# Kernel tuning notes

Hardware: AMD Instinct MI355X
Metric: run time of the kernel (lower is better)

Reference implementation:

```python
import math
import jax, jax.numpy as jnp
import numpy as np

B, T, D = 8, 2048, 512


def setup_inputs() -> dict:
    key = jax.random.key(0)
    kx, = jax.random.split(key, 1)
    x = jax.random.normal(kx, (B, T, D), dtype=jnp.float32)
    log_tau = jnp.asarray(math.log(2.0), dtype=jnp.float32)
    log_blend = jnp.asarray(math.log(0.3 / 0.7), dtype=jnp.float32)
    return {"x": x, "log_tau": log_tau, "log_blend": log_blend}


def _gelu_tanh(x):
    c = math.sqrt(2.0 / math.pi)
    return 0.5 * x * (1.0 + jnp.tanh(c * (x + 0.044715 * x * x * x)))


def reference(x, log_tau, log_blend):
    Bb, Tt, Dd = x.shape
    tau = jnp.exp(log_tau)
    alpha = jax.nn.sigmoid(log_blend)
    # F.normalize(x, dim=-1): divide by L2 norm clamped to eps=1e-12
    norm = jnp.maximum(jnp.linalg.norm(x, axis=-1, keepdims=True), 1e-12)
    x_norm = x / norm
    # cosine self-similarity [B, T, T]
    sim = jnp.einsum("btd,bsd->bts", x_norm, x_norm)
    # triu(diagonal=0) masks j >= i (current + future positions)
    causal_mask = jnp.triu(jnp.ones((Tt, Tt), dtype=bool), k=0)
    sim_causal = jnp.where(causal_mask[None, :, :], -jnp.inf, sim)
    max_sim = jnp.max(sim_causal, axis=-1)  # [B, T]; row 0 is -inf
    max_sim = jnp.nan_to_num(max_sim, nan=0.0, posinf=1.0, neginf=-1.0)
    novelty = jnp.exp(-tau * max_sim)
    scale = (1.0 - alpha + alpha * novelty)[..., None]  # [B, T, 1]
    return _gelu_tanh(x * scale)
```

## Files before the change

kernel.cpp:

```cpp
#include <hip/hip_runtime.h>

#define B_ 8
#define T_ 2048
#define D_ 512

typedef float f32x16 __attribute__((ext_vector_type(16)));
typedef __bf16 bf16x8 __attribute__((ext_vector_type(8)));

__device__ __forceinline__ unsigned encf(float f) {
    int i = __float_as_int(f);
    return (i < 0) ? ~((unsigned)i) : (((unsigned)i) | 0x80000000u);
}
__device__ __forceinline__ float decf(unsigned u) {
    unsigned b = (u & 0x80000000u) ? (u ^ 0x80000000u) : ~u;
    return __int_as_float((int)b);
}

__device__ __forceinline__ void gload_lds16(const char* g, char* l) {
    __builtin_amdgcn_global_load_lds(
        (const __attribute__((address_space(1))) unsigned int*)g,
        (__attribute__((address_space(3))) unsigned int*)l, 16, 0, 0);
}

__global__ __launch_bounds__(256) void pack_kernel(
        const float* __restrict__ x, char* __restrict__ xnp,
        unsigned* __restrict__ msim, float* __restrict__ rnorm) {
    __shared__ __attribute__((aligned(16))) char sP[32768];
    int blk = blockIdx.x;
    int t   = threadIdx.x;
    int ln  = t & 63, w = t >> 6;

#pragma unroll
    for (int q = 0; q < 8; q++) {
        int row32 = q * 4 + w;
        const float* p = x + ((size_t)blk * 32 + row32) * D_ + ln * 8;
        float4 a = *(const float4*)p;
        float4 c = *(const float4*)(p + 4);
        float ss = a.x*a.x + a.y*a.y + a.z*a.z + a.w*a.w
                 + c.x*c.x + c.y*c.y + c.z*c.z + c.w*c.w;
#pragma unroll
        for (int m = 32; m; m >>= 1) ss += __shfl_xor(ss, m);
        if (ln == 0)
            rnorm[blk * 32 + row32] = 1.0f / fmaxf(sqrtf(ss), 1e-12f);
        bf16x8 h;
        h[0] = (__bf16)a.x; h[1] = (__bf16)a.y;
        h[2] = (__bf16)a.z; h[3] = (__bf16)a.w;
        h[4] = (__bf16)c.x; h[5] = (__bf16)c.y;
        h[6] = (__bf16)c.z; h[7] = (__bf16)c.w;
        int ks = ln >> 1, hcw = ln & 1;
        int slot = row32 + hcw * 32;
        int off = ks * 1024 + ((slot * 16) ^ ((ks & 7) << 4));
        *(bf16x8*)(sP + off) = h;
    }
    if (t < 32) msim[blk * 32 + t] = encf(-1e30f);
    __syncthreads();
#pragma unroll
    for (int iq = 0; iq < 8; iq++) {
        int beta = iq * 4096 + t * 16;
        int ks = beta >> 10;
        bf16x8 v = *(const bf16x8*)(sP + ks * 1024 +
                     ((beta & 1023) ^ ((ks & 7) << 4)));
        *(bf16x8*)(xnp + (size_t)blk * 32768 + beta) = v;
    }
}

__global__ __launch_bounds__(256, 2) void simmax_kernel(
        const char* __restrict__ xnp, const float* __restrict__ rnorm,
        unsigned* __restrict__ msim) {
    __shared__ __attribute__((aligned(16))) char sB[16384];

    int bid = blockIdx.x;
    int b   = bid & 7;
    int u   = 71 - (bid >> 3);
    int i = 0, cum = 0;
    while (cum + ((i + 2) >> 1) <= u) { cum += (i + 2) >> 1; i++; }
    int j0 = 2 * (u - cum);

    int t  = threadIdx.x;
    int ln = t & 63, w = t >> 6;
    int wr = w >> 1, wc = w & 1;
    int lr = ln & 31, hc = ln >> 5;
    const float NINF = -__builtin_inff();

    const char*  gA  = xnp + (size_t)(b * 64 + i * 4 + wr * 2) * 32768;
    const float* rnc = rnorm + b * T_;

    f32x16 c00, c01, c10, c11, rm0, rm1;
#pragma unroll
    for (int r = 0; r < 16; r++) {
        c00[r] = 0.f; c01[r] = 0.f; c10[r] = 0.f; c11[r] = 0.f;
        rm0[r] = NINF; rm1[r] = NINF;
    }

    for (int jj = 0; jj < 2; jj++) {
        int j = j0 + jj;
        if (j > i) break;
        const char* gB = xnp + (size_t)(b * 64 + j * 4) * 32768;
        for (int kc = 0; kc < 8; kc++) {
            __syncthreads();
#pragma unroll
            for (int q = 0; q < 4; q++)
                gload_lds16(gB + q * 32768 + (kc * 4 + w) * 1024 + ln * 16,
                            sB + q * 4096 + w * 1024 + ln * 16);
            bf16x8 aF[2][4];
#pragma unroll
            for (int p = 0; p < 2; p++)
#pragma unroll
                for (int ks = 0; ks < 4; ks++)
                    aF[p][ks] = *(const bf16x8*)(gA + p * 32768 +
                                  (kc * 4 + ks) * 1024 + ln * 16);
            __syncthreads();
            const char* bb = sB + (wc * 2) * 4096 + ln * 16;
#pragma unroll
            for (int ks = 0; ks < 4; ks++) {
                bf16x8 b0 = *(const bf16x8*)(bb + ks * 1024);
                bf16x8 b1 = *(const bf16x8*)(bb + 4096 + ks * 1024);
                c00 = __builtin_amdgcn_mfma_f32_32x32x16_bf16(aF[0][ks], b0, c00, 0, 0, 0);
                c01 = __builtin_amdgcn_mfma_f32_32x32x16_bf16(aF[0][ks], b1, c01, 0, 0, 0);
                c10 = __builtin_amdgcn_mfma_f32_32x32x16_bf16(aF[1][ks], b0, c10, 0, 0, 0);
                c11 = __builtin_amdgcn_mfma_f32_32x32x16_bf16(aF[1][ks], b1, c11, 0, 0, 0);
            }
        }
        float rnj0 = rnc[j * 128 + wc * 64 + lr];
        float rnj1 = rnc[j * 128 + wc * 64 + lr + 32];
        bool dt = (j == i);
#pragma unroll
        for (int r = 0; r < 16; r++) {
            int crow = (r & 3) + 8 * (r >> 2) + 4 * hc;
            int cl   = wc * 64 + lr;
            {
                int rloc = wr * 64 + crow;
                float t0 = c00[r] * rnj0, t1 = c01[r] * rnj1;
                if (dt) { if (cl >= rloc) t0 = NINF; if (cl + 32 >= rloc) t1 = NINF; }
                rm0[r] = fmaxf(rm0[r], fmaxf(t0, t1));
                c00[r] = 0.f; c01[r] = 0.f;
            }
            {
                int rloc = wr * 64 + 32 + crow;
                float t0 = c10[r] * rnj0, t1 = c11[r] * rnj1;
                if (dt) { if (cl >= rloc) t0 = NINF; if (cl + 32 >= rloc) t1 = NINF; }
                rm1[r] = fmaxf(rm1[r], fmaxf(t0, t1));
                c10[r] = 0.f; c11[r] = 0.f;
            }
        }
    }

    unsigned* mrow = msim + (size_t)b * T_ + i * 128 + wr * 64;
#pragma unroll
    for (int r = 0; r < 16; r++) {
        int crow = (r & 3) + 8 * (r >> 2) + 4 * hc;
        float v = rm0[r];
        v = fmaxf(v, __shfl_xor(v, 1));
        v = fmaxf(v, __shfl_xor(v, 2));
        v = fmaxf(v, __shfl_xor(v, 4));
        v = fmaxf(v, __shfl_xor(v, 8));
        v = fmaxf(v, __shfl_xor(v, 16));
        if (lr == 0) atomicMax(&mrow[crow], encf(v));
        float v2 = rm1[r];
        v2 = fmaxf(v2, __shfl_xor(v2, 1));
        v2 = fmaxf(v2, __shfl_xor(v2, 2));
        v2 = fmaxf(v2, __shfl_xor(v2, 4));
        v2 = fmaxf(v2, __shfl_xor(v2, 8));
        v2 = fmaxf(v2, __shfl_xor(v2, 16));
        if (lr == 0) atomicMax(&mrow[32 + crow], encf(v2));
    }
}

__global__ __launch_bounds__(256) void gelu_kernel(
        const float* __restrict__ x, const unsigned* __restrict__ msim,
        const float* __restrict__ rnorm,
        const float* __restrict__ ltau, const float* __restrict__ lblend,
        float* __restrict__ out) {
    int i = blockIdx.x * 256 + threadIdx.x;
    float tau   = __expf(ltau[0]);
    float alpha = 1.f / (1.f + __expf(-lblend[0]));
    int row = i >> 7;
    float raw = decf(msim[row]);
    float ms  = (raw < -1e29f) ? -1.0f : raw * rnorm[row];
    float sc = (1.f - alpha) + alpha * __expf(-tau * ms);
    float4 v = ((const float4*)x)[i];
    const float c0 = 0.7978845608028654f;
    const float c1 = 0.044715f;
    float4 o;
#pragma unroll
    for (int k = 0; k < 4; k++) {
        float z = ((const float*)&v)[k] * sc;
        float u = c0 * (z + c1 * z * z * z);
        float e = __expf(2.f * u);
        float th = 1.f - 2.f / (e + 1.f);
        ((float*)&o)[k] = 0.5f * z * (1.f + th);
    }
    ((float4*)out)[i] = o;
}

extern "C" void kernel_launch(void* const* d_in, const int* in_sizes, int n_in,
                              void* d_out, int out_size, void* d_ws, size_t ws_size,
                              hipStream_t stream) {
    (void)in_sizes; (void)n_in; (void)out_size; (void)ws_size;
    const float* x      = (const float*)d_in[0];
    const float* ltau   = (const float*)d_in[1];
    const float* lblend = (const float*)d_in[2];
    float*    out   = (float*)d_out;
    char*     xnp   = (char*)d_out;
    unsigned* msim  = (unsigned*)d_ws;
    float*    rnorm = (float*)((char*)d_ws + 65536);

    pack_kernel<<<B_ * T_ / 32, 256, 0, stream>>>(x, xnp, msim, rnorm);
    simmax_kernel<<<B_ * 72, 256, 0, stream>>>(xnp, rnorm, msim);
    gelu_kernel<<<(B_ * T_ * D_ / 4) / 256, 256, 0, stream>>>(
        x, msim, rnorm, ltau, lblend, out);
}
```

Before: 67.01 us.

## Restructure simmax to stage a full 128-column key tile in LDS

The similarity-max kernel now loads an entire 128-column block of packed keys (all of D) into 128KB of LDS once, with 512-thread blocks. Each wave streams its own 32-row query strip from global memory and runs four MFMA accumulators over the full K dimension without any per-chunk barriers. Work is remapped so each block covers one column tile and up to 256 rows, with a new scheduling formula. This removes the repeated sync/load phases of the old tile loop, at the cost of one block per CU and a large LDS footprint that limits occupancy.

```diff
diff --git a/kernel.cpp b/kernel.cpp
--- a/kernel.cpp
+++ b/kernel.cpp
@@ -64,105 +64,84 @@
     }
 }
 
-__global__ __launch_bounds__(256, 2) void simmax_kernel(
+__global__ __launch_bounds__(512, 1) void simmax_kernel(
         const char* __restrict__ xnp, const float* __restrict__ rnorm,
         unsigned* __restrict__ msim) {
-    __shared__ __attribute__((aligned(16))) char sB[16384];
+    __shared__ __attribute__((aligned(16))) char sB[131072];
 
     int bid = blockIdx.x;
     int b   = bid & 7;
-    int u   = 71 - (bid >> 3);
-    int i = 0, cum = 0;
-    while (cum + ((i + 2) >> 1) <= u) { cum += (i + 2) >> 1; i++; }
-    int j0 = 2 * (u - cum);
+    int u   = bid >> 3;
+    int j, c;
+    if (u >= 64) {
+        int p = u - 64; j = 2 * p + 1; c = 7 - p;
+    } else {
+        j = 0; int acc = 0;
+        while (acc + ((16 - j) >> 1) <= u) { acc += (16 - j) >> 1; j++; }
+        c = u - acc;
+    }
+    int c0  = j * 128;
+    int rp0 = c0 + c * 256;
 
     int t  = threadIdx.x;
     int ln = t & 63, w = t >> 6;
-    int wr = w >> 1, wc = w & 1;
     int lr = ln & 31, hc = ln >> 5;
     const float NINF = -__builtin_inff();
 
-    const char*  gA  = xnp + (size_t)(b * 64 + i * 4 + wr * 2) * 32768;
-    const float* rnc = rnorm + b * T_;
+    const char* gB = xnp + (size_t)(b * 64 + j * 4) * 32768;
+#pragma unroll
+    for (int q = 0; q < 16; q++) {
+        int L = w * 16 + q;
+        gload_lds16(gB + L * 1024 + ln * 16, sB + L * 1024 + ln * 16);
+    }
+    __syncthreads();
 
-    f32x16 c00, c01, c10, c11, rm0, rm1;
+    int myr = rp0 + 32 * w;
+    if (myr < T_) {
+        const char* gA = xnp + (size_t)(b * 64 + (myr >> 5)) * 32768 + ln * 16;
+        const char* lB = sB + ln * 16;
+        f32x16 a0, a1, a2, a3;
 #pragma unroll
-    for (int r = 0; r < 16; r++) {
-        c00[r] = 0.f; c01[r] = 0.f; c10[r] = 0.f; c11[r] = 0.f;
-        rm0[r] = NINF; rm1[r] = NINF;
-    }
+        for (int r = 0; r < 16; r++) { a0[r]=0.f; a1[r]=0.f; a2[r]=0.f; a3[r]=0.f; }
 
-    for (int jj = 0; jj < 2; jj++) {
-        int j = j0 + jj;
-        if (j > i) break;
-        const char* gB = xnp + (size_t)(b * 64 + j * 4) * 32768;
-        for (int kc = 0; kc < 8; kc++) {
-            __syncthreads();
-#pragma unroll
-            for (int q = 0; q < 4; q++)
-                gload_lds16(gB + q * 32768 + (kc * 4 + w) * 1024 + ln * 16,
-                            sB + q * 4096 + w * 1024 + ln * 16);
-            bf16x8 aF[2][4];
-#pragma unroll
-            for (int p = 0; p < 2; p++)
-#pragma unroll
-                for (int ks = 0; ks < 4; ks++)
-                    aF[p][ks] = *(const bf16x8*)(gA + p * 32768 +
-                                  (kc * 4 + ks) * 1024 + ln * 16);
-            __syncthreads();
-            const char* bb = sB + (wc * 2) * 4096 + ln * 16;
-#pragma unroll
-            for (int ks = 0; ks < 4; ks++) {
-                bf16x8 b0 = *(const bf16x8*)(bb + ks * 1024);
-                bf16x8 b1 = *(const bf16x8*)(bb + 4096 + ks * 1024);
-                c00 = __builtin_amdgcn_mfma_f32_32x32x16_bf16(aF[0][ks], b0, c00, 0, 0, 0);
-                c01 = __builtin_amdgcn_mfma_f32_32x32x16_bf16(aF[0][ks], b1, c01, 0, 0, 0);
-                c10 = __builtin_amdgcn_mfma_f32_32x32x16_bf16(aF[1][ks], b0, c10, 0, 0, 0);
-                c11 = __builtin_amdgcn_mfma_f32_32x32x16_bf16(aF[1][ks], b1, c11, 0, 0, 0);
-            }
+#pragma unroll 8
+        for (int k = 0; k < 32; k++) {
+            bf16x8 av = *(const bf16x8*)(gA + k * 1024);
+            bf16x8 b0 = *(const bf16x8*)(lB +          k * 1024);
+            bf16x8 b1 = *(const bf16x8*)(lB + 32768  + k * 1024);
+            bf16x8 b2 = *(const bf16x8*)(lB + 65536  + k * 1024);
+            bf16x8 b3 = *(const bf16x8*)(lB + 98304  + k * 1024);
+            a0 = __builtin_amdgcn_mfma_f32_32x32x16_bf16(av, b0, a0, 0, 0, 0);
+            a1 = __builtin_amdgcn_mfma_f32_32x32x16_bf16(av, b1, a1, 0, 0, 0);
+            a2 = __builtin_amdgcn_mfma_f32_32x32x16_bf16(av, b2, a2, 0, 0, 0);
+            a3 = __builtin_amdgcn_mfma_f32_32x32x16_bf16(av, b3, a3, 0, 0, 0);
         }
-        float rnj0 = rnc[j * 128 + wc * 64 + lr];
-        float rnj1 = rnc[j * 128 + wc * 64 + lr + 32];
-        bool dt = (j == i);
+
+        const float* rnc = rnorm + b * T_;
+        float rn0 = rnc[c0 + lr],      rn1 = rnc[c0 + 32 + lr];
+        float rn2 = rnc[c0 + 64 + lr], rn3 = rnc[c0 + 96 + lr];
+        bool dt = (c0 + 127 >= myr);
+        unsigned* mrow = msim + (size_t)b * T_ + myr;
 #pragma unroll
         for (int r = 0; r < 16; r++) {
             int crow = (r & 3) + 8 * (r >> 2) + 4 * hc;
-            int cl   = wc * 64 + lr;
-            {
-                int rloc = wr * 64 + crow;
-                float t0 = c00[r] * rnj0, t1 = c01[r] * rnj1;
-                if (dt) { if (cl >= rloc) t0 = NINF; if (cl + 32 >= rloc) t1 = NINF; }
-                rm0[r] = fmaxf(rm0[r], fmaxf(t0, t1));
-                c00[r] = 0.f; c01[r] = 0.f;
+            int row  = myr + crow;
+            float t0 = a0[r] * rn0, t1 = a1[r] * rn1;
+            float t2 = a2[r] * rn2, t3 = a3[r] * rn3;
+            if (dt) {
+                if (c0 + lr      >= row) t0 = NINF;
+                if (c0 + 32 + lr >= row) t1 = NINF;
+                if (c0 + 64 + lr >= row) t2 = NINF;
+                if (c0 + 96 + lr >= row) t3 = NINF;
             }
-            {
-                int rloc = wr * 64 + 32 + crow;
-                float t0 = c10[r] * rnj0, t1 = c11[r] * rnj1;
-                if (dt) { if (cl >= rloc) t0 = NINF; if (cl + 32 >= rloc) t1 = NINF; }
-                rm1[r] = fmaxf(rm1[r], fmaxf(t0, t1));
-                c10[r] = 0.f; c11[r] = 0.f;
-            }
+            float v = fmaxf(fmaxf(t0, t1), fmaxf(t2, t3));
+            v = fmaxf(v, __shfl_xor(v, 1));
+            v = fmaxf(v, __shfl_xor(v, 2));
+            v = fmaxf(v, __shfl_xor(v, 4));
+            v = fmaxf(v, __shfl_xor(v, 8));
+            v = fmaxf(v, __shfl_xor(v, 16));
+            if (lr == 0) atomicMax(&mrow[crow], encf(v));
         }
-    }
-
-    unsigned* mrow = msim + (size_t)b * T_ + i * 128 + wr * 64;
-#pragma unroll
-    for (int r = 0; r < 16; r++) {
-        int crow = (r & 3) + 8 * (r >> 2) + 4 * hc;
-        float v = rm0[r];
-        v = fmaxf(v, __shfl_xor(v, 1));
-        v = fmaxf(v, __shfl_xor(v, 2));
-        v = fmaxf(v, __shfl_xor(v, 4));
-        v = fmaxf(v, __shfl_xor(v, 8));
-        v = fmaxf(v, __shfl_xor(v, 16));
-        if (lr == 0) atomicMax(&mrow[crow], encf(v));
-        float v2 = rm1[r];
-        v2 = fmaxf(v2, __shfl_xor(v2, 1));
-        v2 = fmaxf(v2, __shfl_xor(v2, 2));
-        v2 = fmaxf(v2, __shfl_xor(v2, 4));
-        v2 = fmaxf(v2, __shfl_xor(v2, 8));
-        v2 = fmaxf(v2, __shfl_xor(v2, 16));
-        if (lr == 0) atomicMax(&mrow[32 + crow], encf(v2));
     }
 }
 
@@ -206,7 +185,7 @@
     float*    rnorm = (float*)((char*)d_ws + 65536);
 
     pack_kernel<<<B_ * T_ / 32, 256, 0, stream>>>(x, xnp, msim, rnorm);
-    simmax_kernel<<<B_ * 72, 256, 0, stream>>>(xnp, rnorm, msim);
+    simmax_kernel<<<B_ * 72, 512, 0, stream>>>(xnp, rnorm, msim);
     gelu_kernel<<<(B_ * T_ * D_ / 4) / 256, 256, 0, stream>>>(
         x, msim, rnorm, ltau, lblend, out);
 }
```

Measured after the change: 66.32 us. About the same (-1.0%).
